# Kernel optimization log

Measured on AMD Instinct MI355X. Metric: run time of the kernel, lower is better.

Reference implementation:

```python
import jax, jax.numpy as jnp
import numpy as np

NUM_EMBEDDINGS = 1024
EMBEDDING_DIM = 64
SCALE = 1.0 / NUM_EMBEDDINGS


def setup_inputs() -> dict:
    key = jax.random.key(0)
    k1, k2 = jax.random.split(key)
    input = jax.random.normal(k1, (16, EMBEDDING_DIM, 64, 64), dtype=jnp.float32)
    # nn.Embedding weight initialized uniform(-scale, scale)
    codebook = jax.random.uniform(k2, (NUM_EMBEDDINGS, EMBEDDING_DIM),
                                  dtype=jnp.float32, minval=-SCALE, maxval=SCALE)
    return {"input": input, "codebook": codebook}


def reference(input, codebook):
    # NCHW -> NHWC, flatten spatial+batch to tokens [N, D]
    x = jnp.transpose(input, (0, 2, 3, 1))           # [B, H, W, D]
    B, H, W, D = x.shape
    flat = x.reshape(-1, D)                          # [N, D]
    dists = (jnp.sum(flat ** 2, axis=1, keepdims=True)
             + jnp.sum(codebook ** 2, axis=1)
             - 2.0 * flat @ codebook.T)              # [N, K]
    idx = jnp.argmin(dists, axis=-1).reshape(B, H, W)  # [B, H, W]
    quantized = codebook[idx]                        # [B, H, W, D]
    return jnp.transpose(quantized, (0, 3, 1, 2))    # [B, D, H, W]
```

## Files before the change

### kernel.cpp

```cpp
#include <hip/hip_runtime.h>

typedef short short8 __attribute__((ext_vector_type(8)));
typedef float f32x4 __attribute__((ext_vector_type(4)));
typedef unsigned long long u64;

#define NE 1024
#define D 64
#define HW 4096
#define MARGIN 3.0e-3f
#define FLT_MAX_F 3.402823466e+38f
#define MST 33

#define WS_BN  0
#define WS_EBF 4096

__device__ __forceinline__ unsigned short f2bf(float f) {
    unsigned u = __float_as_uint(f);
    return (unsigned short)((u + 0x7fffu + ((u >> 16) & 1u)) >> 16);
}

__device__ __forceinline__ float np_sum64_sq(const float* v) {
    float s[8];
#pragma unroll
    for (int j = 0; j < 8; ++j) s[j] = __fmul_rn(v[j], v[j]);
#pragma unroll
    for (int i = 8; i < 64; i += 8) {
#pragma unroll
        for (int j = 0; j < 8; ++j)
            s[j] = __fadd_rn(s[j], __fmul_rn(v[i + j], v[i + j]));
    }
    return __fadd_rn(__fadd_rn(__fadd_rn(s[0], s[1]), __fadd_rn(s[2], s[3])),
                     __fadd_rn(__fadd_rn(s[4], s[5]), __fadd_rn(s[6], s[7])));
}

__device__ __forceinline__ float np_sum64_sq_str(const float* p) {
    float s[8];
#pragma unroll
    for (int j = 0; j < 8; ++j) { float v = p[j * 128]; s[j] = __fmul_rn(v, v); }
#pragma unroll
    for (int i = 8; i < 64; i += 8) {
#pragma unroll
        for (int j = 0; j < 8; ++j) {
            float v = p[(i + j) * 128];
            s[j] = __fadd_rn(s[j], __fmul_rn(v, v));
        }
    }
    return __fadd_rn(__fadd_rn(__fadd_rn(s[0], s[1]), __fadd_rn(s[2], s[3])),
                     __fadd_rn(__fadd_rn(s[4], s[5]), __fadd_rn(s[6], s[7])));
}

__global__ __launch_bounds__(256) void kP_prep(
        const float* __restrict__ cb, float* __restrict__ bn,
        unsigned short* __restrict__ ebf) {
    const int gid = blockIdx.x * 256 + threadIdx.x;
    ebf[gid] = f2bf(cb[gid]);
    if (gid < NE) {
        float row[D];
        const float4* r4 = reinterpret_cast<const float4*>(cb + (size_t)gid * D);
#pragma unroll
        for (int i = 0; i < 16; ++i) {
            float4 v = r4[i];
            row[4*i+0] = v.x; row[4*i+1] = v.y; row[4*i+2] = v.z; row[4*i+3] = v.w;
        }
        bn[gid] = np_sum64_sq(row);
    }
}

__global__ __launch_bounds__(512, 2) void k_mega(
        const float* __restrict__ in, const unsigned short* __restrict__ ebf,
        const float* __restrict__ bn_g, const float* __restrict__ cb,
        float* __restrict__ out) {
    __shared__ unsigned short ebq[2 * 128 * 64];
    __shared__ float sbn[NE];
    __shared__ unsigned mask32[128 * MST];
    __shared__ unsigned short win_s[128];

    const int tid  = threadIdx.x;
    const int lane = tid & 63, w = tid >> 6;
    const int lcol = lane & 15, lhi = lane >> 4, lrow = lhi * 4;
    const int tokw = blockIdx.x * 128 + w * 16;
    const int b = tokw >> 12, hwb = tokw & 4095;

#pragma unroll
    for (int i = 0; i < 2; ++i)
        sbn[tid + i * 512] = __fmul_rn(-0.5f, bn_g[tid + i * 512]);

    const float* xbase = in + (size_t)b * (D * HW);
    const int hw0 = hwb + lcol;
    const int kb = lhi * 8;
    short8 B00, B01;
    {
        const float* p;
        p = xbase + (size_t)kb * HW + hw0;
#pragma unroll
        for (int j = 0; j < 8; ++j) B00[j] = (short)f2bf(p[(size_t)j * HW]);
        p = xbase + (size_t)(kb + 32) * HW + hw0;
#pragma unroll
        for (int j = 0; j < 8; ++j) B01[j] = (short)f2bf(p[(size_t)j * HW]);
    }

    const int swz   = (lcol & 7) << 4;
    const int aoff0 = lcol * 128 + ((lhi * 16) ^ swz);
    const int aoff1 = lcol * 128 + ((64 + lhi * 16) ^ swz);

    int4 pf0, pf1;
#define LOADC(C) { const int4* s_ = (const int4*)(ebf + (size_t)(C) * 8192);  \
                   pf0 = s_[tid]; pf1 = s_[tid + 512]; }
#define WRITEC(BUF) { int4 t_[2] = {pf0, pf1};                                \
    _Pragma("unroll")                                                         \
    for (int i = 0; i < 2; ++i) {                                             \
        int L = (tid + i * 512) * 16;                                         \
        int row = L >> 7, wi = L & 127;                                       \
        *(int4*)((char*)ebq + (BUF) * 16384 + row * 128                       \
                 + (wi ^ ((row & 7) << 4))) = t_[i];                          \
    } }

#define CHUNK_MFMA(BUF, C, CT)                                                \
    const char* lp = (const char*)ebq + (BUF) * 16384 + (CT) * 2048;          \
    short8 A0 = *(const short8*)(lp + aoff0);                                 \
    short8 A1 = *(const short8*)(lp + aoff1);                                 \
    f32x4 acc = *(const f32x4*)(sbn + (C) * 128 + (CT) * 16 + lrow);          \
    acc = __builtin_amdgcn_mfma_f32_16x16x32_bf16(A0, B00, acc, 0, 0, 0);     \
    acc = __builtin_amdgcn_mfma_f32_16x16x32_bf16(A1, B01, acc, 0, 0, 0);

    f32x4 vA = {-FLT_MAX_F, -FLT_MAX_F, -FLT_MAX_F, -FLT_MAX_F};
    LOADC(0)
    WRITEC(0)
    __syncthreads();
    for (int c = 0; c < 8; ++c) {
        const int buf = c & 1;
        if (c < 7) LOADC(c + 1)
#pragma unroll
        for (int ct = 0; ct < 8; ++ct) {
            CHUNK_MFMA(buf, c, ct)
#pragma unroll
            for (int r = 0; r < 4; ++r) vA[r] = fmaxf(vA[r], acc[r]);
        }
        if (c < 7) WRITEC(buf ^ 1)
        __syncthreads();
    }
    float v0 = fmaxf(fmaxf(vA[0], vA[1]), fmaxf(vA[2], vA[3]));
    v0 = fmaxf(v0, __shfl_xor(v0, 16)); v0 = fmaxf(v0, __shfl_xor(v0, 32));
    const float athr = v0 - 0.5f * MARGIN;
    const int tl = w * 16 + lcol;

    LOADC(0)
    WRITEC(0)
    __syncthreads();
    for (int c = 0; c < 8; ++c) {
        const int buf = c & 1;
        if (c < 7) LOADC(c + 1)
        unsigned m = 0;
#pragma unroll
        for (int ct = 0; ct < 8; ++ct) {
            CHUNK_MFMA(buf, c, ct)
#pragma unroll
            for (int r = 0; r < 4; ++r)
                if (acc[r] >= athr) m |= (1u << (ct * 4 + r));
        }
        mask32[tl * MST + c * 4 + lhi] = m;
        if (c < 7) WRITEC(buf ^ 1)
        __syncthreads();
    }

    float* xshare = (float*)ebq;
    {
        const int hwb0 = (blockIdx.x * 128) & 4095;
        const float* xb0 = in + (size_t)((blockIdx.x * 128) >> 12) * (D * HW) + hwb0;
#pragma unroll
        for (int i = 0; i < 16; ++i) {
            const int idx = i * 512 + tid;
            const int d = idx >> 7, t = idx & 127;
            xshare[d * 128 + t] = xb0[(size_t)d * HW + t];
        }
    }
    __syncthreads();

    {
        const int tok_l = tid >> 2, sub = tid & 3;
        const float* xs = xshare + tok_l;
        const float a = np_sum64_sq_str(xs);

        u64 best = ~0ull;
        int kp = -1;
        int pos = 0;
        for (int w32 = 0; w32 < 32; ++w32) {
            unsigned m = mask32[tok_l * MST + w32];
            const int kbase = (w32 >> 2) * 128 + (w32 & 3) * 4;
            while (m) {
                const int bit = (int)__builtin_ctz(m);
                m &= m - 1;
                const int k = kbase + (bit >> 2) * 16 + (bit & 3);
                if (((pos++) & 3) != sub) continue;
                if (kp < 0) { kp = k; continue; }
                const float4* e0q = reinterpret_cast<const float4*>(cb + (size_t)kp * D);
                const float4* e1q = reinterpret_cast<const float4*>(cb + (size_t)k * D);
                float d0 = 0.f, d1 = 0.f;
#pragma unroll
                for (int i = 0; i < 16; ++i) {
                    float4 a4 = e0q[i], b4 = e1q[i];
                    float x0 = xs[(4*i+0)*128], x1 = xs[(4*i+1)*128];
                    float x2 = xs[(4*i+2)*128], x3 = xs[(4*i+3)*128];
                    d0 = __fmaf_rn(x0, a4.x, d0); d0 = __fmaf_rn(x1, a4.y, d0);
                    d0 = __fmaf_rn(x2, a4.z, d0); d0 = __fmaf_rn(x3, a4.w, d0);
                    d1 = __fmaf_rn(x0, b4.x, d1); d1 = __fmaf_rn(x1, b4.y, d1);
                    d1 = __fmaf_rn(x2, b4.z, d1); d1 = __fmaf_rn(x3, b4.w, d1);
                }
                float q0 = __fsub_rn(__fadd_rn(a, bn_g[kp]), __fmul_rn(2.0f, d0));
                float q1 = __fsub_rn(__fadd_rn(a, bn_g[k]),  __fmul_rn(2.0f, d1));
                u64 key0 = (((u64)__float_as_uint(q0)) << 32) | (unsigned)kp;
                u64 key1 = (((u64)__float_as_uint(q1)) << 32) | (unsigned)k;
                u64 kmin = key0 < key1 ? key0 : key1;
                best = best < kmin ? best : kmin;
                kp = -1;
            }
        }
        if (kp >= 0) {
            const float4* e0q = reinterpret_cast<const float4*>(cb + (size_t)kp * D);
            float d0 = 0.f;
#pragma unroll
            for (int i = 0; i < 16; ++i) {
                float4 a4 = e0q[i];
                d0 = __fmaf_rn(xs[(4*i+0)*128], a4.x, d0);
                d0 = __fmaf_rn(xs[(4*i+1)*128], a4.y, d0);
                d0 = __fmaf_rn(xs[(4*i+2)*128], a4.z, d0);
                d0 = __fmaf_rn(xs[(4*i+3)*128], a4.w, d0);
            }
            float q0 = __fsub_rn(__fadd_rn(a, bn_g[kp]), __fmul_rn(2.0f, d0));
            u64 key0 = (((u64)__float_as_uint(q0)) << 32) | (unsigned)kp;
            best = best < key0 ? best : key0;
        }
#pragma unroll
        for (int o = 1; o < 4; o <<= 1) {
            u64 v = __shfl_xor(best, o);
            best = best < v ? best : v;
        }
        if (sub == 0) win_s[tok_l] = (unsigned short)(best & 0x3FFull);
    }
    __syncthreads();

    {
        const int tok_l = tid >> 2, qd = (tid & 3) << 4;
        const int tok = blockIdx.x * 128 + tok_l;
        const int gb = tok >> 12, ghw = tok & 4095;
        const unsigned k = win_s[tok_l];
        const float4* er = reinterpret_cast<const float4*>(cb + (size_t)k * D + qd);
        float* ot = out + (size_t)gb * (D * HW) + ghw;
#pragma unroll
        for (int i = 0; i < 4; ++i) {
            float4 e = er[i];
            ot[(size_t)(qd + 4*i + 0) * HW] = e.x;
            ot[(size_t)(qd + 4*i + 1) * HW] = e.y;
            ot[(size_t)(qd + 4*i + 2) * HW] = e.z;
            ot[(size_t)(qd + 4*i + 3) * HW] = e.w;
        }
    }
}

extern "C" void kernel_launch(void* const* d_in, const int* in_sizes, int n_in,
                              void* d_out, int out_size, void* d_ws, size_t ws_size,
                              hipStream_t stream) {
    const float* in  = (const float*)d_in[0];
    const float* cb  = (const float*)d_in[1];
    float*       out = (float*)d_out;
    char*        ws  = (char*)d_ws;

    float*          bn  = (float*)(ws + WS_BN);
    unsigned short* ebf = (unsigned short*)(ws + WS_EBF);

    hipLaunchKernelGGL(kP_prep, dim3(256), dim3(256), 0, stream, cb, bn, ebf);
    hipLaunchKernelGGL(k_mega,  dim3(512), dim3(512), 0, stream, in, ebf, bn, cb, out);
}
```

Before: 80.22 us.

## Merge max and mask MFMA passes into one, keep token vector in registers

The two sweeps over the bf16 codebook (one for the max score, one to build the candidate mask) become a single sweep. Each chunk's 32 scores are kept in registers and thresholded against the running max seen so far. This removes a full MFMA pass and its LDS staging. Because early chunks are compared against a looser threshold, they can keep more candidates, which means more exact fp32 refinement work. Separately, each thread now loads its token's 64 input values straight from global memory into registers instead of staging them in LDS, which raises register pressure and duplicates global loads across the 4 threads that share a token.

```diff
diff --git a/kernel.cpp b/kernel.cpp
--- a/kernel.cpp
+++ b/kernel.cpp
@@ -28,22 +28,6 @@
 #pragma unroll
         for (int j = 0; j < 8; ++j)
             s[j] = __fadd_rn(s[j], __fmul_rn(v[i + j], v[i + j]));
-    }
-    return __fadd_rn(__fadd_rn(__fadd_rn(s[0], s[1]), __fadd_rn(s[2], s[3])),
-                     __fadd_rn(__fadd_rn(s[4], s[5]), __fadd_rn(s[6], s[7])));
-}
-
-__device__ __forceinline__ float np_sum64_sq_str(const float* p) {
-    float s[8];
-#pragma unroll
-    for (int j = 0; j < 8; ++j) { float v = p[j * 128]; s[j] = __fmul_rn(v, v); }
-#pragma unroll
-    for (int i = 8; i < 64; i += 8) {
-#pragma unroll
-        for (int j = 0; j < 8; ++j) {
-            float v = p[(i + j) * 128];
-            s[j] = __fadd_rn(s[j], __fmul_rn(v, v));
-        }
     }
     return __fadd_rn(__fadd_rn(__fadd_rn(s[0], s[1]), __fadd_rn(s[2], s[3])),
                      __fadd_rn(__fadd_rn(s[4], s[5]), __fadd_rn(s[6], s[7])));
@@ -115,15 +99,10 @@
                  + (wi ^ ((row & 7) << 4))) = t_[i];                          \
     } }
 
-#define CHUNK_MFMA(BUF, C, CT)                                                \
-    const char* lp = (const char*)ebq + (BUF) * 16384 + (CT) * 2048;          \
-    short8 A0 = *(const short8*)(lp + aoff0);                                 \
-    short8 A1 = *(const short8*)(lp + aoff1);                                 \
-    f32x4 acc = *(const f32x4*)(sbn + (C) * 128 + (CT) * 16 + lrow);          \
-    acc = __builtin_amdgcn_mfma_f32_16x16x32_bf16(A0, B00, acc, 0, 0, 0);     \
-    acc = __builtin_amdgcn_mfma_f32_16x16x32_bf16(A1, B01, acc, 0, 0, 0);
-
     f32x4 vA = {-FLT_MAX_F, -FLT_MAX_F, -FLT_MAX_F, -FLT_MAX_F};
+    const int tl = w * 16 + lcol;
+    float acc32[32];
+
     LOADC(0)
     WRITEC(0)
     __syncthreads();
@@ -132,54 +111,43 @@
         if (c < 7) LOADC(c + 1)
 #pragma unroll
         for (int ct = 0; ct < 8; ++ct) {
-            CHUNK_MFMA(buf, c, ct)
-#pragma unroll
-            for (int r = 0; r < 4; ++r) vA[r] = fmaxf(vA[r], acc[r]);
-        }
-        if (c < 7) WRITEC(buf ^ 1)
-        __syncthreads();
-    }
-    float v0 = fmaxf(fmaxf(vA[0], vA[1]), fmaxf(vA[2], vA[3]));
-    v0 = fmaxf(v0, __shfl_xor(v0, 16)); v0 = fmaxf(v0, __shfl_xor(v0, 32));
-    const float athr = v0 - 0.5f * MARGIN;
-    const int tl = w * 16 + lcol;
-
-    LOADC(0)
-    WRITEC(0)
-    __syncthreads();
-    for (int c = 0; c < 8; ++c) {
-        const int buf = c & 1;
-        if (c < 7) LOADC(c + 1)
+            const char* lp = (const char*)ebq + buf * 16384 + ct * 2048;
+            short8 A0 = *(const short8*)(lp + aoff0);
+            short8 A1 = *(const short8*)(lp + aoff1);
+            f32x4 acc = *(const f32x4*)(sbn + c * 128 + ct * 16 + lrow);
+            acc = __builtin_amdgcn_mfma_f32_16x16x32_bf16(A0, B00, acc, 0, 0, 0);
+            acc = __builtin_amdgcn_mfma_f32_16x16x32_bf16(A1, B01, acc, 0, 0, 0);
+#pragma unroll
+            for (int r = 0; r < 4; ++r) {
+                acc32[ct * 4 + r] = acc[r];
+                vA[r] = fmaxf(vA[r], acc[r]);
+            }
+        }
+        float v0 = fmaxf(fmaxf(vA[0], vA[1]), fmaxf(vA[2], vA[3]));
+        v0 = fmaxf(v0, __shfl_xor(v0, 16));
+        v0 = fmaxf(v0, __shfl_xor(v0, 32));
+        const float athr = v0 - 0.5f * MARGIN;
         unsigned m = 0;
 #pragma unroll
         for (int ct = 0; ct < 8; ++ct) {
-            CHUNK_MFMA(buf, c, ct)
 #pragma unroll
             for (int r = 0; r < 4; ++r)
-                if (acc[r] >= athr) m |= (1u << (ct * 4 + r));
+                if (acc32[ct * 4 + r] >= athr) m |= (1u << (ct * 4 + r));
         }
         mask32[tl * MST + c * 4 + lhi] = m;
         if (c < 7) WRITEC(buf ^ 1)
         __syncthreads();
     }
 
-    float* xshare = (float*)ebq;
-    {
-        const int hwb0 = (blockIdx.x * 128) & 4095;
-        const float* xb0 = in + (size_t)((blockIdx.x * 128) >> 12) * (D * HW) + hwb0;
-#pragma unroll
-        for (int i = 0; i < 16; ++i) {
-            const int idx = i * 512 + tid;
-            const int d = idx >> 7, t = idx & 127;
-            xshare[d * 128 + t] = xb0[(size_t)d * HW + t];
-        }
-    }
-    __syncthreads();
-
     {
         const int tok_l = tid >> 2, sub = tid & 3;
-        const float* xs = xshare + tok_l;
-        const float a = np_sum64_sq_str(xs);
+        const int tok = blockIdx.x * 128 + tok_l;
+        const int tb = tok >> 12, thw = tok & 4095;
+        const float* x = in + (size_t)tb * (D * HW) + thw;
+        float xv[D];
+#pragma unroll
+        for (int d = 0; d < D; ++d) xv[d] = x[(size_t)d * HW];
+        const float a = np_sum64_sq(xv);
 
         u64 best = ~0ull;
         int kp = -1;
@@ -199,8 +167,8 @@
 #pragma unroll
                 for (int i = 0; i < 16; ++i) {
                     float4 a4 = e0q[i], b4 = e1q[i];
-                    float x0 = xs[(4*i+0)*128], x1 = xs[(4*i+1)*128];
-                    float x2 = xs[(4*i+2)*128], x3 = xs[(4*i+3)*128];
+                    float x0 = xv[4*i+0], x1 = xv[4*i+1];
+                    float x2 = xv[4*i+2], x3 = xv[4*i+3];
                     d0 = __fmaf_rn(x0, a4.x, d0); d0 = __fmaf_rn(x1, a4.y, d0);
                     d0 = __fmaf_rn(x2, a4.z, d0); d0 = __fmaf_rn(x3, a4.w, d0);
                     d1 = __fmaf_rn(x0, b4.x, d1); d1 = __fmaf_rn(x1, b4.y, d1);
@@ -221,10 +189,10 @@
 #pragma unroll
             for (int i = 0; i < 16; ++i) {
                 float4 a4 = e0q[i];
-                d0 = __fmaf_rn(xs[(4*i+0)*128], a4.x, d0);
-                d0 = __fmaf_rn(xs[(4*i+1)*128], a4.y, d0);
-                d0 = __fmaf_rn(xs[(4*i+2)*128], a4.z, d0);
-                d0 = __fmaf_rn(xs[(4*i+3)*128], a4.w, d0);
+                d0 = __fmaf_rn(xv[4*i+0], a4.x, d0);
+                d0 = __fmaf_rn(xv[4*i+1], a4.y, d0);
+                d0 = __fmaf_rn(xv[4*i+2], a4.z, d0);
+                d0 = __fmaf_rn(xv[4*i+3], a4.w, d0);
             }
             float q0 = __fsub_rn(__fadd_rn(a, bn_g[kp]), __fmul_rn(2.0f, d0));
             u64 key0 = (((u64)__float_as_uint(q0)) << 32) | (unsigned)kp;
```

After: 153.7 us. 1.92x slower.
